# Kernel tuning notes

Hardware: AMD Instinct MI355X
Metric: run time of the kernel (lower is better)

## Reference

```python
import jax, jax.numpy as jnp
import numpy as np

B, I, H = 16384, 512, 512
HH = H // 2


def _lrelu(v):
    return jnp.where(v > 0, v, 0.01 * v)


def setup_inputs() -> dict:
    key = jax.random.key(0)
    ks = jax.random.split(key, 20)
    s = 1.0 / np.sqrt(H)
    rn = lambda k, shp, sc: (jax.random.normal(k, shp, jnp.float32) * sc)
    return {
        "x": rn(ks[0], (B, I), 1.0),
        "h0": rn(ks[1], (1, B, H), 1.0),
        "c0": rn(ks[2], (1, B, H), 1.0),
        "cum": jax.random.uniform(ks[3], (B, 1), jnp.float32),
        # LSTM params (torch gate order i, f, g, o)
        "W_ih": rn(ks[4], (4 * H, I), s),
        "W_hh": rn(ks[5], (4 * H, H), s),
        "b_ih": rn(ks[6], (4 * H,), s),
        "b_hh": rn(ks[7], (4 * H,), s),
        # skip gate MLP
        "W_sp": rn(ks[8], (HH, H), s),
        "b_sp": rn(ks[9], (HH,), s),
        "W_sc": rn(ks[10], (HH, H), s),
        "b_sc": rn(ks[11], (HH,), s),
        "W_so": rn(ks[12], (1, HH), s),
        "b_so": rn(ks[13], (1,), s),
        # threshold gate MLP
        "W_tp": rn(ks[14], (HH, H), s),
        "b_tp": rn(ks[15], (HH,), s),
        "W_to": rn(ks[16], (1, HH), s),
        "b_to": rn(ks[17], (1,), s),
    }


def reference(x, h0, c0, cum, W_ih, W_hh, b_ih, b_hh,
              W_sp, b_sp, W_sc, b_sc, W_so, b_so,
              W_tp, b_tp, W_to, b_to):
    # single-step, single-layer LSTM
    gates = x @ W_ih.T + b_ih + h0[0] @ W_hh.T + b_hh  # [B, 4H]
    i_g, f_g, g_g, o_g = jnp.split(gates, 4, axis=-1)
    i_g = jax.nn.sigmoid(i_g)
    f_g = jax.nn.sigmoid(f_g)
    g_g = jnp.tanh(g_g)
    o_g = jax.nn.sigmoid(o_g)
    c1l = f_g * c0[0] + i_g * g_g          # [B, H]
    h1l = o_g * jnp.tanh(c1l)              # [B, H]
    h1, c1 = h1l[None], c1l[None]          # [1, B, H]

    # skip gate: delta prob from c0[-1], c1[-1]
    sg = _lrelu(c0[-1] @ W_sp.T + b_sp + c1[-1] @ W_sc.T + b_sc)  # [B, H/2]
    update_prob_delta = jax.nn.sigmoid(sg @ W_so.T + b_so)        # [B, 1]

    # threshold gate from c0[-1]
    tg = _lrelu(c0[-1] @ W_tp.T + b_tp)                           # [B, H/2]
    update_threshold = jax.nn.sigmoid(tg @ W_to.T + b_to)         # [B, 1]

    update_prob = cum + jnp.minimum(update_prob_delta, 1.0 - cum)  # [B, 1]
    # straight-through round: fwd hard threshold, bwd identity to prob
    hard = (update_prob > update_threshold).astype(jnp.float32)
    update_gate = update_prob + jax.lax.stop_gradient(hard - update_prob)

    new_h = update_gate * h1 + (1.0 - update_gate) * h0  # [1, B, H]
    new_c = update_gate * c1 + (1.0 - update_gate) * c0  # [1, B, H]
    update_cum = (1.0 - update_gate) * update_prob        # [B, 1]
    return (new_h, new_c, update_cum, update_prob_delta, update_prob)
```

## Files before the change

### kernel.cpp

```cpp
#include <hip/hip_runtime.h>
#include <math.h>

#define BB 16384
#define HH 512

typedef short short8 __attribute__((ext_vector_type(8)));
typedef float f32x4 __attribute__((ext_vector_type(4)));
typedef unsigned short ushort_t;

__device__ __forceinline__ float sigm(float v){ return 1.0f/(1.0f+expf(-v)); }

__device__ __forceinline__ unsigned short f2bf(float f){
    unsigned int u = __float_as_uint(f);
    u = u + 0x7FFFu + ((u>>16)&1u);
    return (unsigned short)(u>>16);
}
__device__ __forceinline__ float bf2f(unsigned short h){
    return __uint_as_float(((unsigned int)h)<<16);
}
__device__ __forceinline__ void gll16(const void* g, void* l){
    __builtin_amdgcn_global_load_lds((const __attribute__((address_space(1))) void*)g,
                                     (__attribute__((address_space(3))) void*)l, 16, 0, 0);
}

__global__ void k_prep_A(const float* __restrict__ x, const float* __restrict__ h0,
                         ushort_t* __restrict__ A1h, ushort_t* __restrict__ A1l)
{
    int u = blockIdx.x*256 + threadIdx.x;
    int r  = u & 127;
    int c  = (u >> 7) & 3;
    int tk = (u >> 9) & 31;
    int tm = u >> 14;
    int row = tm*128 + r;
    int k0 = tk*32 + c*8;
    const float* src = (k0 < 512) ? (x + (size_t)row*512 + k0)
                                  : (h0 + (size_t)row*512 + (k0-512));
    float4 v0 = *(const float4*)(src);
    float4 v1 = *(const float4*)(src+4);
    float vv[8] = {v0.x,v0.y,v0.z,v0.w,v1.x,v1.y,v1.z,v1.w};
    short8 hi, lo;
#pragma unroll
    for (int j=0;j<8;++j){
        unsigned short h = f2bf(vv[j]);
        unsigned short l = f2bf(vv[j] - bf2f(h));
        hi[j] = (short)h; lo[j] = (short)l;
    }
    size_t off = (size_t)u * 8;
    *(short8*)(A1h + off) = hi;
    *(short8*)(A1l + off) = lo;
}

__global__ void k_prep_A2(const float* __restrict__ c0,
                          ushort_t* __restrict__ A2h, ushort_t* __restrict__ A2l)
{
    int u = blockIdx.x*256 + threadIdx.x;
    int r  = u & 127;
    int c  = (u >> 7) & 3;
    int tk = (u >> 9) & 15;
    int tm = u >> 13;
    int row = tm*128 + r;
    int k0 = tk*32 + c*8;
    const float* src = c0 + (size_t)row*512 + k0;
    float4 v0 = *(const float4*)(src);
    float4 v1 = *(const float4*)(src+4);
    float vv[8] = {v0.x,v0.y,v0.z,v0.w,v1.x,v1.y,v1.z,v1.w};
    short8 hi, lo;
#pragma unroll
    for (int j=0;j<8;++j){
        unsigned short h = f2bf(vv[j]);
        unsigned short l = f2bf(vv[j] - bf2f(h));
        hi[j] = (short)h; lo[j] = (short)l;
    }
    size_t off = ((size_t)tm*32 + tk)*4096 + (size_t)(c*128 + r)*8;
    *(short8*)(A2h + off) = hi;
    *(short8*)(A2l + off) = lo;
}

__global__ void k_prep_B(const float* __restrict__ W_ih, const float* __restrict__ W_hh,
                         const float* __restrict__ b_ih, const float* __restrict__ b_hh,
                         ushort_t* __restrict__ B1h, ushort_t* __restrict__ B1l,
                         float* __restrict__ bgp)
{
    int u = blockIdx.x*256 + threadIdx.x;
    int r  = u & 127;
    int c  = (u >> 7) & 3;
    int tk = (u >> 9) & 31;
    int tn = u >> 14;
    int wcp = r>>6, g=(r>>4)&3, h16 = r&15;
    int h = tn*32 + wcp*16 + h16;
    int wrow = g*512 + h;
    int k0 = tk*32 + c*8;
    const float* src = (k0 < 512) ? (W_ih + (size_t)wrow*512 + k0)
                                  : (W_hh + (size_t)wrow*512 + (k0-512));
    float4 v0 = *(const float4*)(src);
    float4 v1 = *(const float4*)(src+4);
    float vv[8] = {v0.x,v0.y,v0.z,v0.w,v1.x,v1.y,v1.z,v1.w};
    short8 hi, lo;
#pragma unroll
    for (int j=0;j<8;++j){
        unsigned short hq = f2bf(vv[j]);
        unsigned short lq = f2bf(vv[j] - bf2f(hq));
        hi[j] = (short)hq; lo[j] = (short)lq;
    }
    size_t off = (size_t)u * 8;
    *(short8*)(B1h + off) = hi;
    *(short8*)(B1l + off) = lo;
    if (tk == 0 && c == 0) bgp[tn*128 + r] = b_ih[wrow] + b_hh[wrow];
}

__global__ void k_prep_B2(const float* __restrict__ W_sp, const float* __restrict__ W_sc,
                          const float* __restrict__ W_tp,
                          const float* __restrict__ b_sp, const float* __restrict__ b_sc,
                          const float* __restrict__ b_tp,
                          ushort_t* __restrict__ B2h, ushort_t* __restrict__ B2l,
                          float* __restrict__ bs2)
{
    int u = blockIdx.x*256 + threadIdx.x;
    int r  = u & 127;
    int c  = (u >> 7) & 3;
    int tk = (u >> 9) & 31;
    int tn = u >> 14;
    int n = tn*128 + r;
    int k0 = tk*32 + c*8;
    float vv[8];
    if (n < 256) {
        const float* src = (k0 < 512) ? (W_sp + (size_t)n*512 + k0)
                                      : (W_sc + (size_t)n*512 + (k0-512));
        float4 v0 = *(const float4*)(src);
        float4 v1 = *(const float4*)(src+4);
        vv[0]=v0.x; vv[1]=v0.y; vv[2]=v0.z; vv[3]=v0.w;
        vv[4]=v1.x; vv[5]=v1.y; vv[6]=v1.z; vv[7]=v1.w;
    } else if (k0 < 512) {
        const float* src = W_tp + (size_t)(n-256)*512 + k0;
        float4 v0 = *(const float4*)(src);
        float4 v1 = *(const float4*)(src+4);
        vv[0]=v0.x; vv[1]=v0.y; vv[2]=v0.z; vv[3]=v0.w;
        vv[4]=v1.x; vv[5]=v1.y; vv[6]=v1.z; vv[7]=v1.w;
    } else {
#pragma unroll
        for (int j=0;j<8;++j) vv[j] = 0.0f;
    }
    short8 hi, lo;
#pragma unroll
    for (int j=0;j<8;++j){
        unsigned short hq = f2bf(vv[j]);
        unsigned short lq = f2bf(vv[j] - bf2f(hq));
        hi[j] = (short)hq; lo[j] = (short)lq;
    }
    size_t off = (size_t)u * 8;
    *(short8*)(B2h + off) = hi;
    *(short8*)(B2l + off) = lo;
    if (tk == 0 && c == 0) bs2[n] = (n < 256) ? (b_sp[n] + b_sc[n]) : b_tp[n-256];
}

__global__ __launch_bounds__(256) void k_gemm_gates(
    const ushort_t* __restrict__ Ah, const ushort_t* __restrict__ Al,
    const ushort_t* __restrict__ Bh, const ushort_t* __restrict__ Bl,
    const float* __restrict__ bgp, const float* __restrict__ c0,
    float* __restrict__ outH, float* __restrict__ outC,
    ushort_t* __restrict__ A2h, ushort_t* __restrict__ A2l)
{
    __shared__ __align__(16) ushort_t AsH[4096];
    __shared__ __align__(16) ushort_t AsL[4096];
    __shared__ __align__(16) ushort_t BsH[4096];
    __shared__ __align__(16) ushort_t BsL[4096];
    const int tid = threadIdx.x;
    const int lane = tid & 63;
    const int wid = tid >> 6;
    const int wr = wid >> 1, wc = wid & 1;
    const int bid = (int)blockIdx.x;
    const int v = (bid & 7)*256 + (bid >> 3);
    const int tm = v >> 4;
    const int tn = v & 15;
    const int l15 = lane & 15;
    const int lq = lane >> 4;

    f32x4 acc[4][4];
#pragma unroll
    for (int fn = 0; fn < 4; ++fn) {
        float bv = bgp[tn*128 + wc*64 + fn*16 + l15];
#pragma unroll
        for (int fm = 0; fm < 4; ++fm) {
            acc[fm][fn][0]=bv; acc[fm][fn][1]=bv; acc[fm][fn][2]=bv; acc[fm][fn][3]=bv;
        }
    }

    const size_t baseA = (size_t)tm * (32*4096);
    const size_t baseB = (size_t)tn * (32*4096);
    int aoff[4], boff[4];
#pragma unroll
    for (int f = 0; f < 4; ++f) {
        aoff[f] = (lq*128 + wr*64 + f*16 + l15) * 8;
        boff[f] = (lq*128 + wc*64 + f*16 + l15) * 8;
    }
    const int si = wid * 2;

    for (int tk = 0; tk < 32; ++tk) {
        size_t ga = baseA + (size_t)tk*4096 + (size_t)lane*8;
        size_t gb = baseB + (size_t)tk*4096 + (size_t)lane*8;
#pragma unroll
        for (int t = 0; t < 2; ++t) {
            int i = si + t;
            gll16(Ah + ga + i*512, AsH + i*512);
            gll16(Al + ga + i*512, AsL + i*512);
            gll16(Bh + gb + i*512, BsH + i*512);
            gll16(Bl + gb + i*512, BsL + i*512);
        }
        __syncthreads();
        short8 bhv[4], blv[4];
#pragma unroll
        for (int fn = 0; fn < 4; ++fn) {
            bhv[fn] = *(const short8*)&BsH[boff[fn]];
            blv[fn] = *(const short8*)&BsL[boff[fn]];
        }
#pragma unroll
        for (int fm = 0; fm < 4; ++fm) {
            short8 ahv = *(const short8*)&AsH[aoff[fm]];
            short8 alv = *(const short8*)&AsL[aoff[fm]];
#pragma unroll
            for (int fn = 0; fn < 4; ++fn) {
                acc[fm][fn] = __builtin_amdgcn_mfma_f32_16x16x32_bf16(ahv, bhv[fn], acc[fm][fn], 0,0,0);
                acc[fm][fn] = __builtin_amdgcn_mfma_f32_16x16x32_bf16(alv, bhv[fn], acc[fm][fn], 0,0,0);
                acc[fm][fn] = __builtin_amdgcn_mfma_f32_16x16x32_bf16(ahv, blv[fn], acc[fm][fn], 0,0,0);
            }
        }
        __syncthreads();
    }

    const int hb = tn*32 + wc*16;
    const int h = hb + l15;
#pragma unroll
    for (int fm = 0; fm < 4; ++fm) {
        int row0 = tm*128 + wr*64 + fm*16 + lq*4;
#pragma unroll
        for (int r = 0; r < 4; ++r) {
            int row = row0 + r;
            size_t idx = (size_t)row*512 + h;
            float ig = sigm(acc[fm][0][r]);
            float fg = sigm(acc[fm][1][r]);
            float gg = tanhf(acc[fm][2][r]);
            float og = sigm(acc[fm][3][r]);
            float c1 = fg*c0[idx] + ig*gg;
            float h1 = og*tanhf(c1);
            outC[idx] = c1;
            outH[idx] = h1;
            unsigned short ch = f2bf(c1);
            unsigned short cl = f2bf(c1 - bf2f(ch));
            size_t a2 = ((size_t)tm*32 + 16 + tn)*4096
                      + (size_t)((wc*2 + (l15>>3))*128 + (row & 127))*8 + (l15 & 7);
            A2h[a2] = ch;
            A2l[a2] = cl;
        }
    }
}

__global__ __launch_bounds__(256) void k_gemm_sgtg(
    const ushort_t* __restrict__ Ah, const ushort_t* __restrict__ Al,
    const ushort_t* __restrict__ Bh, const ushort_t* __restrict__ Bl,
    const float* __restrict__ bs2,
    float* __restrict__ sgtg)
{
    __shared__ __align__(16) ushort_t AsH[4096];
    __shared__ __align__(16) ushort_t AsL[4096];
    __shared__ __align__(16) ushort_t BsH[4096];
    __shared__ __align__(16) ushort_t BsL[4096];
    const int tid = threadIdx.x;
    const int lane = tid & 63;
    const int wid = tid >> 6;
    const int wr = wid >> 1, wc = wid & 1;
    const int bid = (int)blockIdx.x;
    const int v = (bid & 7)*64 + (bid >> 3);
    const int tm = v >> 2;
    const int tn = v & 3;
    const int l15 = lane & 15;
    const int lq = lane >> 4;

    f32x4 acc[4][4];
#pragma unroll
    for (int fn = 0; fn < 4; ++fn) {
        float bv = bs2[tn*128 + wc*64 + fn*16 + l15];
#pragma unroll
        for (int fm = 0; fm < 4; ++fm) {
            acc[fm][fn][0]=bv; acc[fm][fn][1]=bv; acc[fm][fn][2]=bv; acc[fm][fn][3]=bv;
        }
    }

    const size_t baseA = (size_t)tm * (32*4096);
    const size_t baseB = (size_t)tn * (32*4096);
    int aoff[4], boff[4];
#pragma unroll
    for (int f = 0; f < 4; ++f) {
        aoff[f] = (lq*128 + wr*64 + f*16 + l15) * 8;
        boff[f] = (lq*128 + wc*64 + f*16 + l15) * 8;
    }
    const int si = wid * 2;

    for (int tk = 0; tk < 32; ++tk) {
        size_t ga = baseA + (size_t)tk*4096 + (size_t)lane*8;
        size_t gb = baseB + (size_t)tk*4096 + (size_t)lane*8;
#pragma unroll
        for (int t = 0; t < 2; ++t) {
            int i = si + t;
            gll16(Ah + ga + i*512, AsH + i*512);
            gll16(Al + ga + i*512, AsL + i*512);
            gll16(Bh + gb + i*512, BsH + i*512);
            gll16(Bl + gb + i*512, BsL + i*512);
        }
        __syncthreads();
        short8 bhv[4], blv[4];
#pragma unroll
        for (int fn = 0; fn < 4; ++fn) {
            bhv[fn] = *(const short8*)&BsH[boff[fn]];
            blv[fn] = *(const short8*)&BsL[boff[fn]];
        }
#pragma unroll
        for (int fm = 0; fm < 4; ++fm) {
            short8 ahv = *(const short8*)&AsH[aoff[fm]];
            short8 alv = *(const short8*)&AsL[aoff[fm]];
#pragma unroll
            for (int fn = 0; fn < 4; ++fn) {
                acc[fm][fn] = __builtin_amdgcn_mfma_f32_16x16x32_bf16(ahv, bhv[fn], acc[fm][fn], 0,0,0);
                acc[fm][fn] = __builtin_amdgcn_mfma_f32_16x16x32_bf16(alv, bhv[fn], acc[fm][fn], 0,0,0);
                acc[fm][fn] = __builtin_amdgcn_mfma_f32_16x16x32_bf16(ahv, blv[fn], acc[fm][fn], 0,0,0);
            }
        }
        __syncthreads();
    }

#pragma unroll
    for (int fm = 0; fm < 4; ++fm) {
        int row0 = tm*128 + wr*64 + fm*16 + lq*4;
#pragma unroll
        for (int fn = 0; fn < 4; ++fn) {
            int n = tn*128 + wc*64 + fn*16 + l15;
#pragma unroll
            for (int r = 0; r < 4; ++r) {
                int row = row0 + r;
                float vv = acc[fm][fn][r];
                vv = vv > 0.f ? vv : 0.01f*vv;
                sgtg[(size_t)row*512 + n] = vv;
            }
        }
    }
}

__global__ __launch_bounds__(256) void k_final(
    const float* __restrict__ sgtg,
    const float* __restrict__ h0, const float* __restrict__ c0,
    const float* __restrict__ cum,
    const float* __restrict__ W_so, const float* __restrict__ b_so,
    const float* __restrict__ W_to, const float* __restrict__ b_to,
    float* __restrict__ outH, float* __restrict__ outC,
    float* __restrict__ outCum, float* __restrict__ outDelta, float* __restrict__ outProb)
{
    int w = threadIdx.x >> 6;
    int lane = threadIdx.x & 63;
    int b = blockIdx.x * 4 + w;
    const float* row = sgtg + (size_t)b * 512;
    float so = 0.f, to = 0.f;
#pragma unroll
    for (int u = 0; u < 4; ++u) {
        int c = lane + 64 * u;
        so = fmaf(row[c], W_so[c], so);
        to = fmaf(row[256 + c], W_to[c], to);
    }
#pragma unroll
    for (int off = 32; off; off >>= 1) {
        so += __shfl_down(so, off);
        to += __shfl_down(to, off);
    }
    so = __shfl(so, 0);
    to = __shfl(to, 0);
    float delta = sigm(so + b_so[0]);
    float thr   = sigm(to + b_to[0]);
    float cu = cum[b];
    float prob = cu + fminf(delta, 1.0f - cu);
    float hard = (prob > thr) ? 1.0f : 0.0f;
    if (lane == 0) {
        outDelta[b] = delta;
        outProb[b]  = prob;
        outCum[b]   = (1.0f - hard) * prob;
    }
    if (hard == 0.0f) {
#pragma unroll
        for (int u = 0; u < 8; ++u) {
            size_t idx = (size_t)b * 512 + lane + 64 * u;
            outH[idx] = h0[idx];
            outC[idx] = c0[idx];
        }
    }
}

extern "C" void kernel_launch(void* const* d_in, const int* in_sizes, int n_in,
                              void* d_out, int out_size, void* d_ws, size_t ws_size,
                              hipStream_t stream)
{
    const float* x    = (const float*)d_in[0];
    const float* h0   = (const float*)d_in[1];
    const float* c0   = (const float*)d_in[2];
    const float* cum  = (const float*)d_in[3];
    const float* W_ih = (const float*)d_in[4];
    const float* W_hh = (const float*)d_in[5];
    const float* b_ih = (const float*)d_in[6];
    const float* b_hh = (const float*)d_in[7];
    const float* W_sp = (const float*)d_in[8];
    const float* b_sp = (const float*)d_in[9];
    const float* W_sc = (const float*)d_in[10];
    const float* b_sc = (const float*)d_in[11];
    const float* W_so = (const float*)d_in[12];
    const float* b_so = (const float*)d_in[13];
    const float* W_tp = (const float*)d_in[14];
    const float* b_tp = (const float*)d_in[15];
    const float* W_to = (const float*)d_in[16];
    const float* b_to = (const float*)d_in[17];

    float* out      = (float*)d_out;
    float* outH     = out;
    float* outC     = out + (size_t)BB * HH;
    float* outCum   = out + (size_t)2 * BB * HH;
    float* outDelta = outCum + BB;
    float* outProb  = outDelta + BB;

    char* w = (char*)d_ws;
    ushort_t* A1h = (ushort_t*)(w);
    ushort_t* A1l = (ushort_t*)(w + 33554432ull);
    ushort_t* A2h = (ushort_t*)(w + 67108864ull);
    ushort_t* A2l = (ushort_t*)(w + 100663296ull);
    ushort_t* B1h = (ushort_t*)(w + 134217728ull);
    ushort_t* B1l = (ushort_t*)(w + 138412032ull);
    ushort_t* B2h = (ushort_t*)(w + 142606336ull);
    ushort_t* B2l = (ushort_t*)(w + 143654912ull);
    float*    bgp = (float*)(w + 144703488ull);
    float*    bs2 = (float*)(w + 144711680ull);
    float*    sgtg = (float*)A1h;

    k_prep_A <<<8192, 256, 0, stream>>>(x, h0, A1h, A1l);
    k_prep_A2<<<4096, 256, 0, stream>>>(c0, A2h, A2l);
    k_prep_B <<<1024, 256, 0, stream>>>(W_ih, W_hh, b_ih, b_hh, B1h, B1l, bgp);
    k_prep_B2<<<256, 256, 0, stream>>>(W_sp, W_sc, W_tp, b_sp, b_sc, b_tp, B2h, B2l, bs2);
    k_gemm_gates<<<2048, 256, 0, stream>>>(A1h, A1l, B1h, B1l, bgp, c0,
                                           outH, outC, A2h, A2l);
    k_gemm_sgtg<<<512, 256, 0, stream>>>(A2h, A2l, B2h, B2l, bs2, sgtg);
    k_final<<<4096, 256, 0, stream>>>(sgtg, h0, c0, cum, W_so, b_so, W_to, b_to,
                                      outH, outC, outCum, outDelta, outProb);
}
```

Baseline: 343.9 us.

## Restructure gate GEMM into 256x256 tiles with 4-stage async LDS pipeline

The gates GEMM moves from 128x128 tiles with 256 threads to 256x256 tiles with 512 threads. The three split-bf16 products (hi*hi, lo*hi, hi*lo) are now walked as a single 96-step K loop. Global-to-LDS loads are prefetched three steps ahead into a 4-buffer ring, with explicit barriers, waitcnt and setprio around the MFMA bursts. The prep kernels and the A2 scatter are re-laid out to match the larger tiles. The goal is more data reuse per tile and hiding load latency behind MFMA work, at the cost of 128KB of LDS per block, which lowers occupancy.

```diff
diff --git a/kernel.cpp b/kernel.cpp
--- a/kernel.cpp
+++ b/kernel.cpp
@@ -27,12 +27,12 @@
                          ushort_t* __restrict__ A1h, ushort_t* __restrict__ A1l)
 {
     int u = blockIdx.x*256 + threadIdx.x;
-    int r  = u & 127;
-    int c  = (u >> 7) & 3;
-    int tk = (u >> 9) & 31;
-    int tm = u >> 14;
-    int row = tm*128 + r;
-    int k0 = tk*32 + c*8;
+    int r  = u & 255;
+    int c  = (u >> 8) & 3;
+    int kt = (u >> 10) & 31;
+    int tm = u >> 15;
+    int row = tm*256 + r;
+    int k0 = kt*32 + c*8;
     const float* src = (k0 < 512) ? (x + (size_t)row*512 + k0)
                                   : (h0 + (size_t)row*512 + (k0-512));
     float4 v0 = *(const float4*)(src);
@@ -82,14 +82,14 @@
                          float* __restrict__ bgp)
 {
     int u = blockIdx.x*256 + threadIdx.x;
-    int r  = u & 127;
-    int c  = (u >> 7) & 3;
-    int tk = (u >> 9) & 31;
-    int tn = u >> 14;
-    int wcp = r>>6, g=(r>>4)&3, h16 = r&15;
-    int h = tn*32 + wcp*16 + h16;
+    int r  = u & 255;
+    int c  = (u >> 8) & 3;
+    int kt = (u >> 10) & 31;
+    int tn = u >> 15;
+    int g = (r>>4)&3;
+    int h = tn*64 + (r>>6)*16 + (r&15);
     int wrow = g*512 + h;
-    int k0 = tk*32 + c*8;
+    int k0 = kt*32 + c*8;
     const float* src = (k0 < 512) ? (W_ih + (size_t)wrow*512 + k0)
                                   : (W_hh + (size_t)wrow*512 + (k0-512));
     float4 v0 = *(const float4*)(src);
@@ -105,7 +105,7 @@
     size_t off = (size_t)u * 8;
     *(short8*)(B1h + off) = hi;
     *(short8*)(B1l + off) = lo;
-    if (tk == 0 && c == 0) bgp[tn*128 + r] = b_ih[wrow] + b_hh[wrow];
+    if (kt == 0 && c == 0) bgp[tn*256 + r] = b_ih[wrow] + b_hh[wrow];
 }
 
 __global__ void k_prep_B2(const float* __restrict__ W_sp, const float* __restrict__ W_sc,
@@ -153,85 +153,114 @@
     if (tk == 0 && c == 0) bs2[n] = (n < 256) ? (b_sp[n] + b_sc[n]) : b_tp[n-256];
 }
 
-__global__ __launch_bounds__(256) void k_gemm_gates(
+#define STEP(T, DO_STAGE, VMASM)                                                     \
+  {                                                                                  \
+    ushort_t* bufA = &lds[(T) & 3][0];                                               \
+    ushort_t* bufB = &lds[(T) & 3][8192];                                            \
+    short8 bf[4], af[4];                                                             \
+    _Pragma("unroll") for (int fn = 0; fn < 4; ++fn)                                 \
+        bf[fn] = *(const short8*)&bufB[boff[fn]];                                    \
+    _Pragma("unroll") for (int fm = 0; fm < 4; ++fm)                                 \
+        af[fm] = *(const short8*)&bufA[aoff[fm]];                                    \
+    if (DO_STAGE) {                                                                  \
+        const int uu = (T) + 3;                                                      \
+        const ushort_t* As_ = ((uu >> 5) == 1) ? Al : Ah;                            \
+        size_t ga = ((size_t)tm*32 + (uu & 31))*8192 + (size_t)tid*8;                \
+        ushort_t* dA = &lds[uu & 3][0];                                              \
+        gll16(As_ + ga,        dA + tid*8);                                          \
+        gll16(As_ + ga + 4096, dA + 4096 + tid*8);                                   \
+    }                                                                                \
+    asm volatile("s_barrier" ::: "memory");                                          \
+    asm volatile("s_waitcnt lgkmcnt(0)" ::: "memory");                               \
+    __builtin_amdgcn_sched_barrier(0);                                               \
+    __builtin_amdgcn_s_setprio(1);                                                   \
+    _Pragma("unroll") for (int fm = 0; fm < 4; ++fm)                                 \
+        _Pragma("unroll") for (int fn = 0; fn < 4; ++fn)                             \
+            acc[fm][fn] = __builtin_amdgcn_mfma_f32_16x16x32_bf16(af[fm], bf[fn], acc[fm][fn], 0,0,0); \
+    __builtin_amdgcn_s_setprio(0);                                                   \
+    asm volatile("s_barrier" ::: "memory");                                          \
+    short8 af2[4];                                                                   \
+    _Pragma("unroll") for (int fm = 0; fm < 4; ++fm)                                 \
+        af2[fm] = *(const short8*)&bufA[aoff[4+fm]];                                 \
+    if (DO_STAGE) {                                                                  \
+        const int uu = (T) + 3;                                                      \
+        const ushort_t* Bs_ = ((uu >> 5) == 2) ? Bl : Bh;                            \
+        size_t gb = ((size_t)tn*32 + (uu & 31))*8192 + (size_t)tid*8;                \
+        ushort_t* dB = &lds[uu & 3][8192];                                           \
+        gll16(Bs_ + gb,        dB + tid*8);                                          \
+        gll16(Bs_ + gb + 4096, dB + 4096 + tid*8);                                   \
+    }                                                                                \
+    VMASM;                                                                           \
+    asm volatile("s_barrier" ::: "memory");                                          \
+    asm volatile("s_waitcnt lgkmcnt(0)" ::: "memory");                               \
+    __builtin_amdgcn_sched_barrier(0);                                               \
+    __builtin_amdgcn_s_setprio(1);                                                   \
+    _Pragma("unroll") for (int fm = 0; fm < 4; ++fm)                                 \
+        _Pragma("unroll") for (int fn = 0; fn < 4; ++fn)                             \
+            acc[4+fm][fn] = __builtin_amdgcn_mfma_f32_16x16x32_bf16(af2[fm], bf[fn], acc[4+fm][fn], 0,0,0); \
+    __builtin_amdgcn_s_setprio(0);                                                   \
+    asm volatile("s_barrier" ::: "memory");                                          \
+  }
+
+__global__ __launch_bounds__(512, 2) void k_gemm_gates(
     const ushort_t* __restrict__ Ah, const ushort_t* __restrict__ Al,
     const ushort_t* __restrict__ Bh, const ushort_t* __restrict__ Bl,
     const float* __restrict__ bgp, const float* __restrict__ c0,
     float* __restrict__ outH, float* __restrict__ outC,
     ushort_t* __restrict__ A2h, ushort_t* __restrict__ A2l)
 {
-    __shared__ __align__(16) ushort_t AsH[4096];
-    __shared__ __align__(16) ushort_t AsL[4096];
-    __shared__ __align__(16) ushort_t BsH[4096];
-    __shared__ __align__(16) ushort_t BsL[4096];
-    const int tid = threadIdx.x;
+    __shared__ __align__(16) ushort_t lds[4][16384];
+    const int tid  = threadIdx.x;
     const int lane = tid & 63;
-    const int wid = tid >> 6;
-    const int wr = wid >> 1, wc = wid & 1;
-    const int bid = (int)blockIdx.x;
-    const int v = (bid & 7)*256 + (bid >> 3);
-    const int tm = v >> 4;
-    const int tn = v & 15;
-    const int l15 = lane & 15;
-    const int lq = lane >> 4;
-
-    f32x4 acc[4][4];
+    const int wid  = tid >> 6;
+    const int wr   = wid >> 2;
+    const int wc   = wid & 3;
+    const int l15  = lane & 15;
+    const int lq   = lane >> 4;
+    const int bid  = (int)blockIdx.x;
+    const int v    = (bid & 7)*64 + (bid >> 3);
+    const int tm   = v >> 3;
+    const int tn   = v & 7;
+
+    f32x4 acc[8][4];
 #pragma unroll
     for (int fn = 0; fn < 4; ++fn) {
-        float bv = bgp[tn*128 + wc*64 + fn*16 + l15];
-#pragma unroll
-        for (int fm = 0; fm < 4; ++fm) {
+        float bv = bgp[tn*256 + wc*64 + fn*16 + l15];
+#pragma unroll
+        for (int fm = 0; fm < 8; ++fm) {
             acc[fm][fn][0]=bv; acc[fm][fn][1]=bv; acc[fm][fn][2]=bv; acc[fm][fn][3]=bv;
         }
     }
 
-    const size_t baseA = (size_t)tm * (32*4096);
-    const size_t baseB = (size_t)tn * (32*4096);
-    int aoff[4], boff[4];
-#pragma unroll
-    for (int f = 0; f < 4; ++f) {
-        aoff[f] = (lq*128 + wr*64 + f*16 + l15) * 8;
-        boff[f] = (lq*128 + wc*64 + f*16 + l15) * 8;
-    }
-    const int si = wid * 2;
-
-    for (int tk = 0; tk < 32; ++tk) {
-        size_t ga = baseA + (size_t)tk*4096 + (size_t)lane*8;
-        size_t gb = baseB + (size_t)tk*4096 + (size_t)lane*8;
-#pragma unroll
-        for (int t = 0; t < 2; ++t) {
-            int i = si + t;
-            gll16(Ah + ga + i*512, AsH + i*512);
-            gll16(Al + ga + i*512, AsL + i*512);
-            gll16(Bh + gb + i*512, BsH + i*512);
-            gll16(Bl + gb + i*512, BsL + i*512);
-        }
-        __syncthreads();
-        short8 bhv[4], blv[4];
-#pragma unroll
-        for (int fn = 0; fn < 4; ++fn) {
-            bhv[fn] = *(const short8*)&BsH[boff[fn]];
-            blv[fn] = *(const short8*)&BsL[boff[fn]];
-        }
-#pragma unroll
-        for (int fm = 0; fm < 4; ++fm) {
-            short8 ahv = *(const short8*)&AsH[aoff[fm]];
-            short8 alv = *(const short8*)&AsL[aoff[fm]];
-#pragma unroll
-            for (int fn = 0; fn < 4; ++fn) {
-                acc[fm][fn] = __builtin_amdgcn_mfma_f32_16x16x32_bf16(ahv, bhv[fn], acc[fm][fn], 0,0,0);
-                acc[fm][fn] = __builtin_amdgcn_mfma_f32_16x16x32_bf16(alv, bhv[fn], acc[fm][fn], 0,0,0);
-                acc[fm][fn] = __builtin_amdgcn_mfma_f32_16x16x32_bf16(ahv, blv[fn], acc[fm][fn], 0,0,0);
-            }
-        }
-        __syncthreads();
-    }
-
-    const int hb = tn*32 + wc*16;
-    const int h = hb + l15;
-#pragma unroll
-    for (int fm = 0; fm < 4; ++fm) {
-        int row0 = tm*128 + wr*64 + fm*16 + lq*4;
+    int aoff[8], boff[4];
+#pragma unroll
+    for (int f = 0; f < 8; ++f) aoff[f] = (lq*256 + wr*128 + f*16 + l15) * 8;
+#pragma unroll
+    for (int f = 0; f < 4; ++f) boff[f] = (lq*256 + wc*64 + f*16 + l15) * 8;
+
+#pragma unroll
+    for (int u0 = 0; u0 < 3; ++u0) {
+        size_t ga = ((size_t)tm*32 + u0)*8192 + (size_t)tid*8;
+        size_t gb = ((size_t)tn*32 + u0)*8192 + (size_t)tid*8;
+        gll16(Ah + ga,        &lds[u0][0]     + tid*8);
+        gll16(Ah + ga + 4096, &lds[u0][4096]  + tid*8);
+        gll16(Bh + gb,        &lds[u0][8192]  + tid*8);
+        gll16(Bh + gb + 4096, &lds[u0][12288] + tid*8);
+    }
+    asm volatile("s_waitcnt vmcnt(8)" ::: "memory");
+    asm volatile("s_barrier" ::: "memory");
+
+    for (int t = 0; t < 93; ++t) {
+        STEP(t, 1, asm volatile("s_waitcnt vmcnt(8)" ::: "memory"));
+    }
+    STEP(93, 0, asm volatile("s_waitcnt vmcnt(4)" ::: "memory"));
+    STEP(94, 0, asm volatile("s_waitcnt vmcnt(0)" ::: "memory"));
+    STEP(95, 0, ((void)0));
+
+    const int h = tn*64 + wc*16 + l15;
+#pragma unroll
+    for (int fm = 0; fm < 8; ++fm) {
+        int row0 = tm*256 + wr*128 + fm*16 + lq*4;
 #pragma unroll
         for (int r = 0; r < 4; ++r) {
             int row = row0 + r;
@@ -246,8 +275,8 @@
             outH[idx] = h1;
             unsigned short ch = f2bf(c1);
             unsigned short cl = f2bf(c1 - bf2f(ch));
-            size_t a2 = ((size_t)tm*32 + 16 + tn)*4096
-                      + (size_t)((wc*2 + (l15>>3))*128 + (row & 127))*8 + (l15 & 7);
+            size_t a2 = ((size_t)(row>>7)*32 + 16 + (h>>5))*4096
+                      + (size_t)((((h>>3)&3))*128 + (row&127))*8 + (h&7);
             A2h[a2] = ch;
             A2l[a2] = cl;
         }
@@ -438,8 +467,8 @@
     k_prep_A2<<<4096, 256, 0, stream>>>(c0, A2h, A2l);
     k_prep_B <<<1024, 256, 0, stream>>>(W_ih, W_hh, b_ih, b_hh, B1h, B1l, bgp);
     k_prep_B2<<<256, 256, 0, stream>>>(W_sp, W_sc, W_tp, b_sp, b_sc, b_tp, B2h, B2l, bs2);
-    k_gemm_gates<<<2048, 256, 0, stream>>>(A1h, A1l, B1h, B1l, bgp, c0,
-                                           outH, outC, A2h, A2l);
+    k_gemm_gates<<<512, 512, 0, stream>>>(A1h, A1l, B1h, B1l, bgp, c0,
+                                          outH, outC, A2h, A2l);
     k_gemm_sgtg<<<512, 256, 0, stream>>>(A2h, A2l, B2h, B2l, bs2, sgtg);
     k_final<<<4096, 256, 0, stream>>>(sgtg, h0, c0, cum, W_so, b_so, W_to, b_to,
                                       outH, outC, outCum, outDelta, outProb);
```

Measured after the change: 349.2 us. No clear change (+1.5%).
